# Optimization experiments

Hardware: AMD Instinct MI355X
Metric: run time of the kernel (lower is better)

Reference implementation:

```python
import jax, jax.numpy as jnp
from jax import lax
import numpy as np

K = 10            # size_feat
N_MU = 10         # number of mean-PSF components
NCH = K * K + N_MU  # 110 depthwise channels
KLEN = 65         # precomputed kernel length


def setup_inputs() -> dict:
    key = jax.random.key(0)
    ks = jax.random.split(key, 12)
    B, C, H, W = 1, 3, 256, 256
    img = jax.random.uniform(ks[0], (B, C, H, W), jnp.float32)
    zernike = jax.random.normal(ks[1], (B, H, W, 35), jnp.float32)
    # pos displacements (first 2 channels) scaled to a few pixels
    zernike = zernike.at[..., :2].multiply(2.0)
    fc1_w = jax.random.normal(ks[2], (200, 33), jnp.float32) / np.float32(np.sqrt(33))
    fc1_b = jax.random.normal(ks[3], (200,), jnp.float32) * 0.01
    fc2_w = jax.random.normal(ks[4], (200, 200), jnp.float32) / np.float32(np.sqrt(200))
    fc2_b = jax.random.normal(ks[5], (200,), jnp.float32) * 0.01
    fc3_w = jax.random.normal(ks[6], (100, 200), jnp.float32) * 0.01
    fc3_b = jnp.zeros((100,), jnp.float32)
    basis_left = jax.random.normal(ks[7], (KLEN, K), jnp.float32) * 0.05
    basis_right = jax.random.normal(ks[8], (KLEN, K), jnp.float32) * 0.05
    mu = jax.random.uniform(ks[9], (KLEN, N_MU), jnp.float32) / np.float32(KLEN)
    return dict(img=img, zernike=zernike, fc1_w=fc1_w, fc1_b=fc1_b,
                fc2_w=fc2_w, fc2_b=fc2_b, fc3_w=fc3_w, fc3_b=fc3_b,
                basis_left=basis_left, basis_right=basis_right, mu=mu, ksize=65)


def _grid_sample_border(img, pos):
    """Bilinear grid_sample, padding_mode='border', align_corners=False.
    img: (B,C,H,W), pos: (B,H,W,2) pixel displacements (x,y)."""
    B, C, H, W = img.shape
    yy, xx = jnp.meshgrid(jnp.arange(H, dtype=jnp.float32),
                          jnp.arange(W, dtype=jnp.float32), indexing='ij')
    grid = jnp.stack((xx, yy), -1)                       # (H,W,2)
    wh = jnp.array([W - 1, H - 1], jnp.float32)
    flow = 2.0 * (grid[None] + pos) / wh - 1.0           # (B,H,W,2) in [-1,1]
    ix = ((flow[..., 0] + 1.0) * W - 1.0) * 0.5
    iy = ((flow[..., 1] + 1.0) * H - 1.0) * 0.5
    ix = jnp.clip(ix, 0.0, W - 1)
    iy = jnp.clip(iy, 0.0, H - 1)
    x0 = jnp.floor(ix); y0 = jnp.floor(iy)
    wx = ix - x0;       wy = iy - y0
    x0i = jnp.clip(x0.astype(jnp.int32), 0, W - 1)
    y0i = jnp.clip(y0.astype(jnp.int32), 0, H - 1)
    x1i = jnp.clip(x0i + 1, 0, W - 1)
    y1i = jnp.clip(y0i + 1, 0, H - 1)

    def bilerp(im, x0i, x1i, y0i, y1i, wx, wy):
        g = lambda yi, xi: im[:, yi, xi]                 # (C,H,W)
        top = g(y0i, x0i) * (1 - wx) + g(y0i, x1i) * wx
        bot = g(y1i, x0i) * (1 - wx) + g(y1i, x1i) * wx
        return top * (1 - wy) + bot * wy

    return jax.vmap(bilerp)(img, x0i, x1i, y0i, y1i, wx, wy)


def _depthwise(x, w, pad_axis, pad):
    # x: (N, NCH, H, W); w: (NCH,1,kh,kw). Reflect 'same' padding on pad_axis.
    cfg = [(0, 0)] * 4
    cfg[pad_axis] = (pad, pad)
    xp = jnp.pad(x, cfg, mode='reflect')
    return lax.conv_general_dilated(
        xp, w, (1, 1), 'VALID',
        dimension_numbers=('NCHW', 'OIHW', 'NCHW'),
        feature_group_count=x.shape[1])


def _forward(img, zernike, fc1_w, fc1_b, fc2_w, fc2_b, fc3_w, fc3_b,
             basis_left, basis_right, mu, ksize):
    B, C, H, W = img.shape
    pad = ksize // 2
    # --- grid-sample warp ---
    tilt = _grid_sample_border(img, zernike[..., :2])    # (B,C,H,W)
    # --- per-pixel MLP -> PSF coefficients ---
    f = zernike[..., 2:]                                  # (B,H,W,33)
    h = jax.nn.leaky_relu(f @ fc1_w.T + fc1_b)
    h = jax.nn.leaky_relu(h @ fc2_w.T + fc2_b)
    coef = h @ fc3_w.T + fc3_b                            # (B,H,W,100)
    weight = jnp.concatenate(
        [coef, jnp.ones((B, H, W, N_MU), coef.dtype)], -1)  # (B,H,W,110)
    # --- elementwise weight multiply ---
    big = jnp.concatenate([tilt, jnp.ones_like(tilt)], 1)  # (B,2C,H,W)
    big = big[..., None] * weight[:, None]                 # (B,2C,H,W,110)
    x = big.reshape(B * 2 * C, H, W, NCH).transpose(0, 3, 1, 2)  # (B*2C,110,H,W)
    # --- separable depthwise blur kernels (outer products Z_i x X_j + mu) ---
    wl = jnp.concatenate([jnp.repeat(basis_left.T, K, axis=0), mu.T], 0)  # (110,klen)
    wr = jnp.concatenate([jnp.tile(basis_right.T, (K, 1)), mu.T], 0)      # (110,klen)
    wl = wl[:, None, :, None]                              # (110,1,klen,1)
    wr = wr[:, None, None, :]                              # (110,1,1,klen)
    y = _depthwise(x, wl, 2, pad)
    y = _depthwise(y, wr, 3, pad)
    d = y.reshape(B, 2 * C, NCH, H, W)
    out = jnp.sum(d[:, :3], axis=2) / jnp.sum(d[:, 3:], axis=2)  # (B,3,H,W)
    return out


def reference(img, zernike, fc1_w, fc1_b, fc2_w, fc2_b, fc3_w, fc3_b,
              basis_left, basis_right, mu, ksize):
    return _forward(img, zernike, fc1_w, fc1_b, fc2_w, fc2_b, fc3_w, fc3_b,
                    basis_left, basis_right, mu, ksize)
```

## Files before the change

### kernel.cpp

```cpp
#include <hip/hip_runtime.h>

#define HW 65536

typedef __attribute__((ext_vector_type(8))) short short8;
typedef __attribute__((ext_vector_type(4))) float float4v;

__device__ __forceinline__ int refl(int i){ if (i < 0) i = -i; if (i > 255) i = 510 - i; return i; }
__device__ __forceinline__ float lrelu(float x){ return x > 0.f ? x : 0.01f * x; }
__device__ __forceinline__ unsigned int f2bf(float x){
  union { float f; unsigned int u; } v; v.f = x;
  unsigned int r = v.u + 0x7fff + ((v.u >> 16) & 1);
  return r >> 16;
}

__global__ __launch_bounds__(256) void k_gridsample(const float* __restrict__ img,
                                                    const float* __restrict__ zern,
                                                    float* __restrict__ tilt){
  int x = threadIdx.x, y = blockIdx.x;
  int pix = y * 256 + x;
  float px = zern[pix * 35 + 0], py = zern[pix * 35 + 1];
  float ix = ((float)x + px) * (256.f / 255.f) - 0.5f;
  float iy = ((float)y + py) * (256.f / 255.f) - 0.5f;
  ix = fminf(fmaxf(ix, 0.f), 255.f);
  iy = fminf(fmaxf(iy, 0.f), 255.f);
  float x0f = floorf(ix), y0f = floorf(iy);
  float wx = ix - x0f, wy = iy - y0f;
  int x0 = (int)x0f, y0 = (int)y0f;
  int x1 = min(x0 + 1, 255), y1 = min(y0 + 1, 255);
  #pragma unroll
  for (int c = 0; c < 3; ++c){
    const float* im = img + c * HW;
    float g00 = im[y0 * 256 + x0], g01 = im[y0 * 256 + x1];
    float g10 = im[y1 * 256 + x0], g11 = im[y1 * 256 + x1];
    float top = g00 * (1.f - wx) + g01 * wx;
    float bot = g10 * (1.f - wx) + g11 * wx;
    tilt[c * HW + pix] = top * (1.f - wy) + bot * wy;
  }
}

#define W2OFF 13312
#define W3OFF 59904
__global__ __launch_bounds__(256) void k_wcvt(const float* __restrict__ w1,
    const float* __restrict__ w2, const float* __restrict__ w3,
    unsigned short* __restrict__ wbf){
  int i = blockIdx.x * 256 + threadIdx.x;
  if (i < 208 * 64){
    int n = i >> 6, k = i & 63;
    float v = (n < 200 && k < 33) ? w1[n * 33 + k] : 0.f;
    wbf[i] = (unsigned short)f2bf(v);
  } else if (i < W2OFF + 208 * 224){
    int j = i - W2OFF; int n = j / 224, k = j - n * 224;
    float v = (n < 200 && k < 200) ? w2[n * 200 + k] : 0.f;
    wbf[i] = (unsigned short)f2bf(v);
  } else if (i < 84992){
    int j = i - W3OFF; int n = j / 224, k = j - n * 224;
    float v = (n < 100 && k < 200) ? w3[n * 200 + k] : 0.f;
    wbf[i] = (unsigned short)f2bf(v);
  }
}

__global__ __launch_bounds__(256) void k_tz(const float* __restrict__ bl,
    const float* __restrict__ mu, unsigned short* __restrict__ Tt){
  int e = blockIdx.x * 256 + threadIdx.x;
  if (e >= 30720) return;
  int t = e / 1536, rem = e - t * 1536;
  int m = rem / 96, k = rem - m * 96;
  int d = k - m;
  float v = 0.f;
  if (d >= 0 && d <= 64) v = (t < 10) ? bl[d * 10 + t] : mu[d * 10 + (t - 10)];
  Tt[e] = (unsigned short)f2bf(v);
}

#define HSTR 232
__global__ __launch_bounds__(256, 1) void k_mlp(const float* __restrict__ zern,
    const float* __restrict__ b1f, const float* __restrict__ b2f,
    const float* __restrict__ b3f, const unsigned short* __restrict__ wbf,
    float* __restrict__ coefp){
  __shared__ char smem[59392];
  unsigned short* H1 = (unsigned short*)smem;
  float*          H3 = (float*)smem;
  unsigned short* XB = (unsigned short*)(smem + 29696);
  unsigned short* H2 = XB;
  int tid = threadIdx.x;
  int pix0 = blockIdx.x * 64;
  int lane = tid & 63, wv = tid >> 6;
  int ln = lane & 15, qd = lane >> 4;

  for (int e = tid; e < 2304; e += 256) ((int*)XB)[e] = 0;
  for (int e = tid; e < 768; e += 256){
    int m = e / 12, j = e - m * 12;
    ((int*)H1)[m * 116 + 104 + j] = 0;
  }
  __syncthreads();
  for (int e = tid; e < 64 * 33; e += 256){
    int m = e / 33, k = e - m * 33;
    XB[m * 72 + k] = (unsigned short)f2bf(zern[(pix0 + m) * 35 + 2 + k]);
  }
  __syncthreads();

  for (int nt = wv; nt < 13; nt += 4){
    int n = nt * 16 + ln;
    short8 b0 = *(const short8*)(wbf + n * 64 + qd * 8);
    short8 b1 = *(const short8*)(wbf + n * 64 + 32 + qd * 8);
    float bv = (n < 200) ? b1f[n] : 0.f;
    #pragma unroll
    for (int mt = 0; mt < 4; ++mt){
      float4v acc = {bv, bv, bv, bv};
      short8 a0 = *(const short8*)(XB + (mt * 16 + ln) * 72 + qd * 8);
      short8 a1 = *(const short8*)(XB + (mt * 16 + ln) * 72 + 32 + qd * 8);
      acc = __builtin_amdgcn_mfma_f32_16x16x32_bf16(a0, b0, acc, 0, 0, 0);
      acc = __builtin_amdgcn_mfma_f32_16x16x32_bf16(a1, b1, acc, 0, 0, 0);
      #pragma unroll
      for (int r = 0; r < 4; ++r)
        H1[(mt * 16 + qd * 4 + r) * HSTR + n] = (unsigned short)f2bf(lrelu(acc[r]));
    }
  }
  __syncthreads();

  for (int e = tid; e < 768; e += 256){
    int m = e / 12, j = e - m * 12;
    ((int*)H2)[m * 116 + 104 + j] = 0;
  }
  {
    const unsigned short* w2p = wbf + W2OFF;
    for (int nt = wv; nt < 13; nt += 4){
      int n = nt * 16 + ln;
      short8 bf[7];
      #pragma unroll
      for (int kc = 0; kc < 7; ++kc)
        bf[kc] = *(const short8*)(w2p + n * 224 + kc * 32 + qd * 8);
      float bv = (n < 200) ? b2f[n] : 0.f;
      #pragma unroll
      for (int mt = 0; mt < 4; ++mt){
        float4v acc = {bv, bv, bv, bv};
        #pragma unroll
        for (int kc = 0; kc < 7; ++kc){
          short8 af = *(const short8*)(H1 + (mt * 16 + ln) * HSTR + kc * 32 + qd * 8);
          acc = __builtin_amdgcn_mfma_f32_16x16x32_bf16(af, bf[kc], acc, 0, 0, 0);
        }
        #pragma unroll
        for (int r = 0; r < 4; ++r)
          H2[(mt * 16 + qd * 4 + r) * HSTR + n] = (unsigned short)f2bf(lrelu(acc[r]));
      }
    }
  }
  __syncthreads();

  {
    const unsigned short* w3p = wbf + W3OFF;
    for (int nt = wv; nt < 7; nt += 4){
      int n = nt * 16 + ln;
      short8 bf[7];
      #pragma unroll
      for (int kc = 0; kc < 7; ++kc)
        bf[kc] = *(const short8*)(w3p + n * 224 + kc * 32 + qd * 8);
      float bv = (n < 100) ? b3f[n] : 0.f;
      #pragma unroll
      for (int mt = 0; mt < 4; ++mt){
        float4v acc = {bv, bv, bv, bv};
        #pragma unroll
        for (int kc = 0; kc < 7; ++kc){
          short8 af = *(const short8*)(H2 + (mt * 16 + ln) * HSTR + kc * 32 + qd * 8);
          acc = __builtin_amdgcn_mfma_f32_16x16x32_bf16(af, bf[kc], acc, 0, 0, 0);
        }
        #pragma unroll
        for (int r = 0; r < 4; ++r)
          H3[(mt * 16 + qd * 4 + r) * 113 + n] = acc[r];
      }
    }
  }
  __syncthreads();

  for (int e = tid; e < 100 * 64; e += 256){
    int n = e >> 6, m = e & 63;
    coefp[n * HW + pix0 + m] = H3[m * 113 + n];
  }
}

#define VB 344
__global__ __launch_bounds__(256) void k_vconv10(const float* __restrict__ tilt,
    const float* __restrict__ coefp, const unsigned short* __restrict__ Tt,
    float* __restrict__ sbuf, float* __restrict__ smu){
  __shared__ __align__(16) unsigned short sxb[16 * VB];
  int tid = threadIdx.x;
  int bid = blockIdx.x;
  int lane = tid & 63, wv = tid >> 6;
  int ln = lane & 15, qd = lane >> 4;
  int col = tid & 15, seg = tid >> 4;
  int r0 = seg * 20;

  int goff[20];
  #pragma unroll
  for (int q = 0; q < 20; ++q) goff[q] = refl(r0 + q - 32) * 256 + col;

  for (int e = tid; e < 384; e += 256){
    int cc = e / 24, rp = e - cc * 24;
    sxb[cc * VB + 320 + rp] = 0;
  }

  if (bid < 640){
    int s = bid & 15;
    int cj = bid >> 4;
    int c = cj / 10, j = cj - c * 10;
    int x0 = s * 16;
    float treg[20];
    if (c < 3){
      const float* tc = tilt + c * HW + x0;
      #pragma unroll
      for (int q = 0; q < 20; ++q) treg[q] = tc[goff[q]];
    }
    float pf[20];
    {
      const float* cq = coefp + j * HW + x0;
      #pragma unroll
      for (int q = 0; q < 20; ++q) pf[q] = cq[goff[q]];
    }
    float4v acc[4];
    #pragma unroll
    for (int t = 0; t < 4; ++t) acc[t] = (float4v){0.f, 0.f, 0.f, 0.f};
    for (int i = 0; i < 10; ++i){
      __syncthreads();
      #pragma unroll
      for (int q = 0; q < 10; ++q){
        float v0 = pf[2 * q], v1 = pf[2 * q + 1];
        if (c < 3){ v0 *= treg[2 * q]; v1 *= treg[2 * q + 1]; }
        unsigned int pk = f2bf(v0) | (f2bf(v1) << 16);
        *(unsigned int*)&sxb[col * VB + r0 + 2 * q] = pk;
      }
      __syncthreads();
      if (i < 9){
        const float* cn = coefp + ((i + 1) * 10 + j) * HW + x0;
        #pragma unroll
        for (int q = 0; q < 20; ++q) pf[q] = cn[goff[q]];
      }
      const unsigned short* ta = Tt + i * 1536 + ln * 96 + qd * 8;
      short8 A0 = *(const short8*)(ta);
      short8 A1 = *(const short8*)(ta + 32);
      short8 A2 = *(const short8*)(ta + 64);
      #pragma unroll
      for (int t = 0; t < 4; ++t){
        int yt = wv * 4 + t;
        const unsigned short* bp = sxb + ln * VB + yt * 16 + qd * 8;
        short8 B0 = *(const short8*)(bp);
        short8 B1 = *(const short8*)(bp + 32);
        short8 B2 = *(const short8*)(bp + 64);
        acc[t] = __builtin_amdgcn_mfma_f32_16x16x32_bf16(A0, B0, acc[t], 0, 0, 0);
        acc[t] = __builtin_amdgcn_mfma_f32_16x16x32_bf16(A1, B1, acc[t], 0, 0, 0);
        acc[t] = __builtin_amdgcn_mfma_f32_16x16x32_bf16(A2, B2, acc[t], 0, 0, 0);
      }
    }
    float* S = sbuf + (c * 10 + j) * HW + x0 + ln;
    #pragma unroll
    for (int t = 0; t < 4; ++t){
      int yt = wv * 4 + t;
      #pragma unroll
      for (int r = 0; r < 4; ++r)
        S[(yt * 16 + qd * 4 + r) * 256] = acc[t][r];
    }
  } else {
    int b2 = bid - 640;
    int c = b2 >> 4, s = b2 & 15;
    int x0 = s * 16;
    const float* tc = tilt + c * HW + x0;
    float tv[20];
    #pragma unroll
    for (int q = 0; q < 20; ++q) tv[q] = tc[goff[q]];
    #pragma unroll
    for (int q = 0; q < 10; ++q){
      unsigned int pk = f2bf(tv[2 * q]) | (f2bf(tv[2 * q + 1]) << 16);
      *(unsigned int*)&sxb[col * VB + r0 + 2 * q] = pk;
    }
    __syncthreads();
    for (int m = 0; m < 10; ++m){
      const unsigned short* ta = Tt + (10 + m) * 1536 + ln * 96 + qd * 8;
      short8 A0 = *(const short8*)(ta);
      short8 A1 = *(const short8*)(ta + 32);
      short8 A2 = *(const short8*)(ta + 64);
      float4v acc[4];
      #pragma unroll
      for (int t = 0; t < 4; ++t) acc[t] = (float4v){0.f, 0.f, 0.f, 0.f};
      #pragma unroll
      for (int t = 0; t < 4; ++t){
        int yt = wv * 4 + t;
        const unsigned short* bp = sxb + ln * VB + yt * 16 + qd * 8;
        short8 B0 = *(const short8*)(bp);
        short8 B1 = *(const short8*)(bp + 32);
        short8 B2 = *(const short8*)(bp + 64);
        acc[t] = __builtin_amdgcn_mfma_f32_16x16x32_bf16(A0, B0, acc[t], 0, 0, 0);
        acc[t] = __builtin_amdgcn_mfma_f32_16x16x32_bf16(A1, B1, acc[t], 0, 0, 0);
        acc[t] = __builtin_amdgcn_mfma_f32_16x16x32_bf16(A2, B2, acc[t], 0, 0, 0);
      }
      float* S = smu + (c * 10 + m) * HW + x0 + ln;
      #pragma unroll
      for (int t = 0; t < 4; ++t){
        int yt = wv * 4 + t;
        #pragma unroll
        for (int r = 0; r < 4; ++r)
          S[(yt * 16 + qd * 4 + r) * 256] = acc[t][r];
      }
    }
  }
}

__global__ __launch_bounds__(256) void k_hconv5(const float* __restrict__ sbuf,
    const float* __restrict__ smu, const float* __restrict__ br,
    const float* __restrict__ mu, float* __restrict__ part){
  __shared__ __align__(16) float sr[4][320];
  int tid = threadIdx.x;
  int grp = blockIdx.x >> 6;
  int yt = blockIdx.x & 63;
  int r = tid >> 6, xg = tid & 63, x0 = xg * 4;
  int isbr = (grp < 8);
  int tgt, h;
  if (isbr){ tgt = grp >> 1; h = grp & 1; }
  else     { int g2 = grp - 8; tgt = g2 >> 1; h = g2 & 1; }
  const float* kp   = isbr ? br : mu;
  const float* base = isbr ? (sbuf + tgt * 10 * HW) : (smu + tgt * 10 * HW);
  float a0 = 0.f, a1 = 0.f, a2 = 0.f, a3 = 0.f;
  for (int p = 0; p < 5; ++p){
    int col = h * 5 + p;
    const float* plane = base + col * HW;
    __syncthreads();
    for (int e = tid; e < 1280; e += 256){
      int rr = e / 320, ii = e - rr * 320;
      sr[rr][ii] = plane[(yt * 4 + rr) * 256 + refl(ii - 32)];
    }
    __syncthreads();
    float4 av = *(const float4*)&sr[r][x0];
    for (int u = 0; u < 64; u += 4){
      float4 bv = *(const float4*)&sr[r][x0 + u + 4];
      float k0 = kp[u * 10 + col],       k1 = kp[(u + 1) * 10 + col],
            k2 = kp[(u + 2) * 10 + col], k3 = kp[(u + 3) * 10 + col];
      a0 += k0 * av.x + k1 * av.y + k2 * av.z + k3 * av.w;
      a1 += k0 * av.y + k1 * av.z + k2 * av.w + k3 * bv.x;
      a2 += k0 * av.z + k1 * av.w + k2 * bv.x + k3 * bv.y;
      a3 += k0 * av.w + k1 * bv.x + k2 * bv.y + k3 * bv.z;
      av = bv;
    }
    float k64 = kp[640 + col];
    a0 += k64 * av.x; a1 += k64 * av.y; a2 += k64 * av.z; a3 += k64 * av.w;
  }
  float4 res = {a0, a1, a2, a3};
  *(float4*)(part + grp * HW + (yt * 4 + r) * 256 + x0) = res;
}

__global__ __launch_bounds__(256) void k_final(const float* __restrict__ part,
                                               const float* __restrict__ mu,
                                               float* __restrict__ out){
  int pix = blockIdx.x * 256 + threadIdx.x;
  float muC = 0.f;
  #pragma unroll
  for (int m = 0; m < 10; ++m){
    float s = 0.f;
    for (int u = 0; u < 65; ++u) s += mu[u * 10 + m];
    muC += s * s;
  }
  float den = part[6 * HW + pix] + part[7 * HW + pix] + muC;
  float inv = 1.f / den;
  #pragma unroll
  for (int c = 0; c < 3; ++c){
    float num = part[(2 * c) * HW + pix] + part[(2 * c + 1) * HW + pix]
              + part[(8 + 2 * c) * HW + pix] + part[(9 + 2 * c) * HW + pix];
    out[c * HW + pix] = num * inv;
  }
}

extern "C" void kernel_launch(void* const* d_in, const int* in_sizes, int n_in,
                              void* d_out, int out_size, void* d_ws, size_t ws_size,
                              hipStream_t stream) {
  const float* img  = (const float*)d_in[0];
  const float* zern = (const float*)d_in[1];
  const float* w1   = (const float*)d_in[2];
  const float* b1   = (const float*)d_in[3];
  const float* w2   = (const float*)d_in[4];
  const float* b2   = (const float*)d_in[5];
  const float* w3   = (const float*)d_in[6];
  const float* b3   = (const float*)d_in[7];
  const float* bl   = (const float*)d_in[8];
  const float* br   = (const float*)d_in[9];
  const float* mu   = (const float*)d_in[10];
  float* out = (float*)d_out;

  float* w     = (float*)d_ws;
  float* tilt  = w;
  float* coefp = w + 3 * HW;
  float* part  = w + 3 * HW;
  float* sbuf  = w + 103 * HW;
  float* smu   = w + 143 * HW;
  unsigned short* wbf = (unsigned short*)sbuf;
  unsigned short* Tt  = (unsigned short*)(w + 173 * HW);

  k_gridsample<<<256, 256, 0, stream>>>(img, zern, tilt);
  k_wcvt<<<332, 256, 0, stream>>>(w1, w2, w3, wbf);
  k_tz<<<120, 256, 0, stream>>>(bl, mu, Tt);
  k_mlp<<<1024, 256, 0, stream>>>(zern, b1, b2, b3, wbf, coefp);
  k_vconv10<<<688, 256, 0, stream>>>(tilt, coefp, Tt, sbuf, smu);
  k_hconv5<<<896, 256, 0, stream>>>(sbuf, smu, br, mu, part);
  k_final<<<256, 256, 0, stream>>>(part, mu, out);
}
```

Measured before the change: 184.0 us.

## Move horizontal blur to bf16 MFMA Toeplitz GEMM and halve MLP tile

The horizontal 65-tap convolution pass is rewritten from scalar fp32 FMAs into bf16 MFMA matrix multiplies. It uses Toeplitz matrices built from basis_right in the extended k_tz table, and each block now processes a 16x256 row tile. Separately, the MLP kernel processes 32 pixels per block instead of 64, halving shared memory and dropping the launch_bounds occupancy restriction so more blocks can be resident. The horizontal pass now rounds intermediates to bf16, which adds precision error compared with the previous fp32 path.

```diff
diff --git a/kernel.cpp b/kernel.cpp
--- a/kernel.cpp
+++ b/kernel.cpp
@@ -60,39 +60,44 @@
 }
 
 __global__ __launch_bounds__(256) void k_tz(const float* __restrict__ bl,
-    const float* __restrict__ mu, unsigned short* __restrict__ Tt){
+    const float* __restrict__ br, const float* __restrict__ mu,
+    unsigned short* __restrict__ Tt){
   int e = blockIdx.x * 256 + threadIdx.x;
-  if (e >= 30720) return;
+  if (e >= 46080) return;
   int t = e / 1536, rem = e - t * 1536;
   int m = rem / 96, k = rem - m * 96;
   int d = k - m;
   float v = 0.f;
-  if (d >= 0 && d <= 64) v = (t < 10) ? bl[d * 10 + t] : mu[d * 10 + (t - 10)];
+  if (d >= 0 && d <= 64){
+    if (t < 10)      v = bl[d * 10 + t];
+    else if (t < 20) v = mu[d * 10 + (t - 10)];
+    else             v = br[d * 10 + (t - 20)];
+  }
   Tt[e] = (unsigned short)f2bf(v);
 }
 
 #define HSTR 232
-__global__ __launch_bounds__(256, 1) void k_mlp(const float* __restrict__ zern,
+__global__ __launch_bounds__(256) void k_mlp(const float* __restrict__ zern,
     const float* __restrict__ b1f, const float* __restrict__ b2f,
     const float* __restrict__ b3f, const unsigned short* __restrict__ wbf,
     float* __restrict__ coefp){
-  __shared__ char smem[59392];
+  __shared__ char smem[29696];
   unsigned short* H1 = (unsigned short*)smem;
   float*          H3 = (float*)smem;
-  unsigned short* XB = (unsigned short*)(smem + 29696);
+  unsigned short* XB = (unsigned short*)(smem + 14848);
   unsigned short* H2 = XB;
   int tid = threadIdx.x;
-  int pix0 = blockIdx.x * 64;
+  int pix0 = blockIdx.x * 32;
   int lane = tid & 63, wv = tid >> 6;
   int ln = lane & 15, qd = lane >> 4;
 
-  for (int e = tid; e < 2304; e += 256) ((int*)XB)[e] = 0;
-  for (int e = tid; e < 768; e += 256){
+  for (int e = tid; e < 1152; e += 256) ((int*)XB)[e] = 0;
+  for (int e = tid; e < 384; e += 256){
     int m = e / 12, j = e - m * 12;
     ((int*)H1)[m * 116 + 104 + j] = 0;
   }
   __syncthreads();
-  for (int e = tid; e < 64 * 33; e += 256){
+  for (int e = tid; e < 32 * 33; e += 256){
     int m = e / 33, k = e - m * 33;
     XB[m * 72 + k] = (unsigned short)f2bf(zern[(pix0 + m) * 35 + 2 + k]);
   }
@@ -104,7 +109,7 @@
     short8 b1 = *(const short8*)(wbf + n * 64 + 32 + qd * 8);
     float bv = (n < 200) ? b1f[n] : 0.f;
     #pragma unroll
-    for (int mt = 0; mt < 4; ++mt){
+    for (int mt = 0; mt < 2; ++mt){
       float4v acc = {bv, bv, bv, bv};
       short8 a0 = *(const short8*)(XB + (mt * 16 + ln) * 72 + qd * 8);
       short8 a1 = *(const short8*)(XB + (mt * 16 + ln) * 72 + 32 + qd * 8);
@@ -117,7 +122,7 @@
   }
   __syncthreads();
 
-  for (int e = tid; e < 768; e += 256){
+  for (int e = tid; e < 384; e += 256){
     int m = e / 12, j = e - m * 12;
     ((int*)H2)[m * 116 + 104 + j] = 0;
   }
@@ -131,7 +136,7 @@
         bf[kc] = *(const short8*)(w2p + n * 224 + kc * 32 + qd * 8);
       float bv = (n < 200) ? b2f[n] : 0.f;
       #pragma unroll
-      for (int mt = 0; mt < 4; ++mt){
+      for (int mt = 0; mt < 2; ++mt){
         float4v acc = {bv, bv, bv, bv};
         #pragma unroll
         for (int kc = 0; kc < 7; ++kc){
@@ -156,7 +161,7 @@
         bf[kc] = *(const short8*)(w3p + n * 224 + kc * 32 + qd * 8);
       float bv = (n < 100) ? b3f[n] : 0.f;
       #pragma unroll
-      for (int mt = 0; mt < 4; ++mt){
+      for (int mt = 0; mt < 2; ++mt){
         float4v acc = {bv, bv, bv, bv};
         #pragma unroll
         for (int kc = 0; kc < 7; ++kc){
@@ -171,8 +176,8 @@
   }
   __syncthreads();
 
-  for (int e = tid; e < 100 * 64; e += 256){
-    int n = e >> 6, m = e & 63;
+  for (int e = tid; e < 3200; e += 256){
+    int n = e >> 5, m = e & 31;
     coefp[n * HW + pix0 + m] = H3[m * 113 + n];
   }
 }
@@ -302,46 +307,68 @@
   }
 }
 
-__global__ __launch_bounds__(256) void k_hconv5(const float* __restrict__ sbuf,
-    const float* __restrict__ smu, const float* __restrict__ br,
-    const float* __restrict__ mu, float* __restrict__ part){
-  __shared__ __align__(16) float sr[4][320];
+#define HS2 328
+__global__ __launch_bounds__(256) void k_hconv8(const float* __restrict__ sbuf,
+    const float* __restrict__ smu, const unsigned short* __restrict__ Tt,
+    float* __restrict__ part){
+  __shared__ __align__(16) unsigned short sxb[16 * HS2];
   int tid = threadIdx.x;
-  int grp = blockIdx.x >> 6;
-  int yt = blockIdx.x & 63;
-  int r = tid >> 6, xg = tid & 63, x0 = xg * 4;
+  int grp = blockIdx.x >> 4;
+  int yt  = blockIdx.x & 15;
+  int y0 = yt * 16;
+  int lane = tid & 63, wv = tid >> 6;
+  int ln = lane & 15, qd = lane >> 4;
+  int srow = tid >> 4, scol = tid & 15;
   int isbr = (grp < 8);
   int tgt, h;
   if (isbr){ tgt = grp >> 1; h = grp & 1; }
   else     { int g2 = grp - 8; tgt = g2 >> 1; h = g2 & 1; }
-  const float* kp   = isbr ? br : mu;
   const float* base = isbr ? (sbuf + tgt * 10 * HW) : (smu + tgt * 10 * HW);
-  float a0 = 0.f, a1 = 0.f, a2 = 0.f, a3 = 0.f;
+  int tbase = isbr ? 20 : 10;
+
+  int gx[20];
+  #pragma unroll
+  for (int q = 0; q < 20; ++q) gx[q] = refl(scol * 20 - 32 + q);
+
+  float4v acc[4];
+  #pragma unroll
+  for (int t = 0; t < 4; ++t) acc[t] = (float4v){0.f, 0.f, 0.f, 0.f};
+
   for (int p = 0; p < 5; ++p){
     int col = h * 5 + p;
-    const float* plane = base + col * HW;
+    const float* plane = base + col * HW + (y0 + srow) * 256;
     __syncthreads();
-    for (int e = tid; e < 1280; e += 256){
-      int rr = e / 320, ii = e - rr * 320;
-      sr[rr][ii] = plane[(yt * 4 + rr) * 256 + refl(ii - 32)];
+    float v[20];
+    #pragma unroll
+    for (int q = 0; q < 20; ++q) v[q] = plane[gx[q]];
+    #pragma unroll
+    for (int q = 0; q < 10; ++q){
+      unsigned int pk = f2bf(v[2 * q]) | (f2bf(v[2 * q + 1]) << 16);
+      *(unsigned int*)&sxb[srow * HS2 + scol * 20 + 2 * q] = pk;
     }
     __syncthreads();
-    float4 av = *(const float4*)&sr[r][x0];
-    for (int u = 0; u < 64; u += 4){
-      float4 bv = *(const float4*)&sr[r][x0 + u + 4];
-      float k0 = kp[u * 10 + col],       k1 = kp[(u + 1) * 10 + col],
-            k2 = kp[(u + 2) * 10 + col], k3 = kp[(u + 3) * 10 + col];
-      a0 += k0 * av.x + k1 * av.y + k2 * av.z + k3 * av.w;
-      a1 += k0 * av.y + k1 * av.z + k2 * av.w + k3 * bv.x;
-      a2 += k0 * av.z + k1 * av.w + k2 * bv.x + k3 * bv.y;
-      a3 += k0 * av.w + k1 * bv.x + k2 * bv.y + k3 * bv.z;
-      av = bv;
-    }
-    float k64 = kp[640 + col];
-    a0 += k64 * av.x; a1 += k64 * av.y; a2 += k64 * av.z; a3 += k64 * av.w;
-  }
-  float4 res = {a0, a1, a2, a3};
-  *(float4*)(part + grp * HW + (yt * 4 + r) * 256 + x0) = res;
+    const unsigned short* ta = Tt + (tbase + col) * 1536 + ln * 96 + qd * 8;
+    short8 A0 = *(const short8*)(ta);
+    short8 A1 = *(const short8*)(ta + 32);
+    short8 A2 = *(const short8*)(ta + 64);
+    #pragma unroll
+    for (int t = 0; t < 4; ++t){
+      int wt = wv * 4 + t;
+      const unsigned short* bp = sxb + ln * HS2 + wt * 16 + qd * 8;
+      short8 B0 = *(const short8*)(bp);
+      short8 B1 = *(const short8*)(bp + 32);
+      short8 B2 = *(const short8*)(bp + 64);
+      acc[t] = __builtin_amdgcn_mfma_f32_16x16x32_bf16(A0, B0, acc[t], 0, 0, 0);
+      acc[t] = __builtin_amdgcn_mfma_f32_16x16x32_bf16(A1, B1, acc[t], 0, 0, 0);
+      acc[t] = __builtin_amdgcn_mfma_f32_16x16x32_bf16(A2, B2, acc[t], 0, 0, 0);
+    }
+  }
+  #pragma unroll
+  for (int t = 0; t < 4; ++t){
+    int wt = wv * 4 + t;
+    float4 res = {acc[t][0], acc[t][1], acc[t][2], acc[t][3]};
+    *(float4*)(part + grp * HW + (y0 + ln) * 256 + wt * 16 + qd * 4) = res;
+  }
 }
 
 __global__ __launch_bounds__(256) void k_final(const float* __restrict__ part,
@@ -392,9 +419,9 @@
 
   k_gridsample<<<256, 256, 0, stream>>>(img, zern, tilt);
   k_wcvt<<<332, 256, 0, stream>>>(w1, w2, w3, wbf);
-  k_tz<<<120, 256, 0, stream>>>(bl, mu, Tt);
-  k_mlp<<<1024, 256, 0, stream>>>(zern, b1, b2, b3, wbf, coefp);
+  k_tz<<<180, 256, 0, stream>>>(bl, br, mu, Tt);
+  k_mlp<<<2048, 256, 0, stream>>>(zern, b1, b2, b3, wbf, coefp);
   k_vconv10<<<688, 256, 0, stream>>>(tilt, coefp, Tt, sbuf, smu);
-  k_hconv5<<<896, 256, 0, stream>>>(sbuf, smu, br, mu, part);
+  k_hconv8<<<224, 256, 0, stream>>>(sbuf, smu, Tt, part);
   k_final<<<256, 256, 0, stream>>>(part, mu, out);
 }
```

New measurement: 170.9 us. 7.1% less time.
